# Kernel optimization log

Measured on AMD Instinct MI355X. Metric: run time of the kernel, lower is better.

The kernel has to match this reference:

```python
import jax, jax.numpy as jnp
import numpy as np

S, B, L, D, H, NOP = 4, 8, 512, 128, 128, 64  # segments, batch, seg_len, input_dim, hidden, n_operators
W = S * L  # 2048 total words
FT = 0.1   # forget-gate floor


def _norm_mat(m):
    # divide each row by its count of nonzero entries (torch normalize_matrix)
    cnt = (m != 0).sum(-1, keepdims=True).astype(m.dtype)
    return m / (cnt + 1e-30)


def _l2(x):
    return x / (jnp.linalg.norm(x, axis=-1, keepdims=True) + 1e-30)


def setup_inputs() -> dict:
    key = jax.random.key(0)
    ks = jax.random.split(key, 16)
    word_outputs = jax.random.normal(ks[0], (S, B, L, D), jnp.float32)
    node_hidden = jax.random.normal(ks[1], (B, D), jnp.float32)
    op_embedding = jax.random.normal(ks[2], (B, NOP, D), jnp.float32)
    word_operator = (jax.random.uniform(ks[3], (B, W, NOP)) < 0.05).astype(jnp.float32)
    word_word = (jax.random.uniform(ks[4], (B, W, W)) < 0.02).astype(jnp.float32)
    depend_relation = (jax.random.uniform(ks[5], (S, B, L, L)) < 0.05).astype(jnp.float32)
    word_exist_matrix = (jax.random.uniform(ks[6], (B, W, W)) < 0.9).astype(jnp.float32)
    word_exist_sequence = (jax.random.uniform(ks[7], (B, W)) < 0.9).astype(jnp.float32)
    goal_word = (jax.random.uniform(ks[8], (B, W)) < 0.2).astype(jnp.float32)

    def lin(k, fi, fo):
        k1, k2 = jax.random.split(k)
        s = 1.0 / np.sqrt(fi).astype(np.float32)
        return (jax.random.uniform(k1, (fi, fo), jnp.float32, -s, s),
                jax.random.uniform(k2, (fo,), jnp.float32, -s, s))

    o_w_W, o_w_b = lin(ks[9], D, H)
    wk_W, wk_b = lin(ks[10], D, H)
    ws_W, ws_b = lin(ks[11], D, H)
    up_W, up_b = lin(ks[12], 3 * H, D)
    wg_W, wg_b = lin(ks[13], D, D)
    fg_W, fg_b = lin(ks[14], 2 * D, D)
    return dict(word_outputs=word_outputs, node_hidden=node_hidden, op_embedding=op_embedding,
                word_operator=word_operator, word_word=word_word, depend_relation=depend_relation,
                word_exist_matrix=word_exist_matrix, word_exist_sequence=word_exist_sequence,
                goal_word=goal_word, o_w_W=o_w_W, o_w_b=o_w_b, wk_W=wk_W, wk_b=wk_b,
                ws_W=ws_W, ws_b=ws_b, up_W=up_W, up_b=up_b, wg_W=wg_W, wg_b=wg_b,
                fg_W=fg_W, fg_b=fg_b)


def reference(word_outputs, node_hidden, op_embedding, word_operator, word_word,
              depend_relation, word_exist_matrix, word_exist_sequence, goal_word,
              o_w_W, o_w_b, wk_W, wk_b, ws_W, ws_b, up_W, up_b, wg_W, wg_b, fg_W, fg_b):
    # cat(word_outputs, dim=1) -> [B, W, D]
    all_word = word_outputs.transpose(1, 0, 2, 3).reshape(B, W, D)
    # operator aggregation: [B,W,NOP] @ o_w(op_embedding) -> [B,W,H], L2-normalized
    word_o = _l2(jnp.einsum('bwo,boh->bwh', word_operator, op_embedding @ o_w_W + o_w_b))
    # knowledge aggregation over masked word-word adjacency
    adj_k = _norm_mat(word_word * word_exist_matrix)
    word_w_k = _l2(jnp.einsum('bvw,bwh->bvh', adj_k, all_word @ wk_W + wk_b))
    # per-segment dependency aggregation, then concat along word dim
    seg = jnp.einsum('sbij,sbjh->sbih', _norm_mat(depend_relation), word_outputs @ ws_W + ws_b)
    word_w_s = _l2(seg.transpose(1, 0, 2, 3).reshape(B, W, H))
    neighbor = jnp.concatenate([word_o, word_w_k, word_w_s], axis=-1)  # [B, W, 3H]
    word_updated = jax.nn.relu(neighbor @ up_W + up_b)  # [B, W, D]
    # goal pooling: bmm([B,1,W],[B,W,D]) -> [B,D]
    gw = _norm_mat(goal_word * word_exist_sequence)
    goal_w = jnp.einsum('bw,bwd->bd', gw, word_updated)
    goal_updated = jax.nn.relu(goal_w @ wg_W + wg_b)
    forget = jax.nn.sigmoid(jnp.concatenate([goal_w, node_hidden], axis=-1) @ fg_W + fg_b)
    return jnp.maximum(forget, FT) * node_hidden + (1.0 - forget) * goal_updated
```

## Files before the change

### kernel.cpp

```cpp
#include <hip/hip_runtime.h>
#include <math.h>

#define Sn 4
#define Bn 8
#define Ln 512
#define Dn 128
#define Hn 128
#define NOPn 64
#define Wn 2048


__device__ __forceinline__ float bf2f(unsigned short u) {
    return __uint_as_float(((unsigned int)u) << 16);
}
__device__ __forceinline__ unsigned short f2bf(float f) {
    unsigned int u = __float_as_uint(f);
    return (unsigned short)((u + 0x7FFFu + ((u >> 16) & 1u)) >> 16);
}

__global__ __launch_bounds__(256) void prep_k(const float* __restrict__ A,
                                              const float* __restrict__ W1,
                                              const float* __restrict__ W2,
                                              const float* __restrict__ b1,
                                              const float* __restrict__ b2,
                                              unsigned short* __restrict__ C1,
                                              unsigned short* __restrict__ C2,
                                              const float* __restrict__ ope,
                                              const float* __restrict__ owW,
                                              const float* __restrict__ owb,
                                              unsigned short* __restrict__ oph,
                                              const float* __restrict__ goal,
                                              const float* __restrict__ wes,
                                              int* __restrict__ widx,
                                              int* __restrict__ wcnt,
                                              float* __restrict__ gwacc) {
    __shared__ __align__(16) float lA[32][68];
    __shared__ __align__(16) float lW1[32][132];
    __shared__ __align__(16) float lW2[32][132];
    __shared__ int cnt;
    const int bid = blockIdx.x, tid = threadIdx.x;

    if (bid < 256) {
        const int m0 = bid * 64;
        float acc1[4][8] = {}, acc2[4][8] = {};
        const int r0 = (tid & 15) * 4;
        const int h0 = (tid >> 4) * 8;
        for (int k0 = 0; k0 < 128; k0 += 32) {
            __syncthreads();
            {
                const int r = tid >> 2, kk = (tid & 3) * 8;
                const float* src = A + (size_t)(m0 + r) * 128 + (k0 + kk);
                float4 v0 = reinterpret_cast<const float4*>(src)[0];
                float4 v1 = reinterpret_cast<const float4*>(src)[1];
                lA[kk + 0][r] = v0.x; lA[kk + 1][r] = v0.y;
                lA[kk + 2][r] = v0.z; lA[kk + 3][r] = v0.w;
                lA[kk + 4][r] = v1.x; lA[kk + 5][r] = v1.y;
                lA[kk + 6][r] = v1.z; lA[kk + 7][r] = v1.w;
            }
            {
                const int kk = tid >> 3, hh = (tid & 7) * 16;
                const float* s1 = W1 + (size_t)(k0 + kk) * 128 + hh;
                const float* s2 = W2 + (size_t)(k0 + kk) * 128 + hh;
#pragma unroll
                for (int q = 0; q < 4; ++q) {
                    float4 v1 = reinterpret_cast<const float4*>(s1)[q];
                    float4 v2 = reinterpret_cast<const float4*>(s2)[q];
                    lW1[kk][hh + 4 * q + 0] = v1.x; lW1[kk][hh + 4 * q + 1] = v1.y;
                    lW1[kk][hh + 4 * q + 2] = v1.z; lW1[kk][hh + 4 * q + 3] = v1.w;
                    lW2[kk][hh + 4 * q + 0] = v2.x; lW2[kk][hh + 4 * q + 1] = v2.y;
                    lW2[kk][hh + 4 * q + 2] = v2.z; lW2[kk][hh + 4 * q + 3] = v2.w;
                }
            }
            __syncthreads();
#pragma unroll
            for (int k = 0; k < 32; ++k) {
                float4 a   = *reinterpret_cast<const float4*>(&lA[k][r0]);
                float4 w10 = *reinterpret_cast<const float4*>(&lW1[k][h0]);
                float4 w11 = *reinterpret_cast<const float4*>(&lW1[k][h0 + 4]);
                float4 w20 = *reinterpret_cast<const float4*>(&lW2[k][h0]);
                float4 w21 = *reinterpret_cast<const float4*>(&lW2[k][h0 + 4]);
                float av[4] = {a.x, a.y, a.z, a.w};
                float wv1[8] = {w10.x, w10.y, w10.z, w10.w, w11.x, w11.y, w11.z, w11.w};
                float wv2[8] = {w20.x, w20.y, w20.z, w20.w, w21.x, w21.y, w21.z, w21.w};
#pragma unroll
                for (int i = 0; i < 4; ++i)
#pragma unroll
                    for (int j = 0; j < 8; ++j) {
                        acc1[i][j] = fmaf(av[i], wv1[j], acc1[i][j]);
                        acc2[i][j] = fmaf(av[i], wv2[j], acc2[i][j]);
                    }
            }
        }
#pragma unroll
        for (int i = 0; i < 4; ++i) {
            alignas(16) unsigned short u1[8], u2[8];
#pragma unroll
            for (int j = 0; j < 8; ++j) {
                u1[j] = f2bf(acc1[i][j] + b1[h0 + j]);
                u2[j] = f2bf(acc2[i][j] + b2[h0 + j]);
            }
            const size_t off = (size_t)(m0 + r0 + i) * 128 + h0;
            *reinterpret_cast<uint4*>(C1 + off) = *reinterpret_cast<const uint4*>(u1);
            *reinterpret_cast<uint4*>(C2 + off) = *reinterpret_cast<const uint4*>(u2);
        }
    } else if (bid < 264) {
        const int m0 = (bid - 256) * 64;
        float acc[4][8] = {};
        const int r0 = (tid & 15) * 4;
        const int h0 = (tid >> 4) * 8;
        for (int k0 = 0; k0 < 128; k0 += 32) {
            __syncthreads();
            {
                const int r = tid >> 2, kk = (tid & 3) * 8;
                const float* src = ope + (size_t)(m0 + r) * 128 + (k0 + kk);
                float4 v0 = reinterpret_cast<const float4*>(src)[0];
                float4 v1 = reinterpret_cast<const float4*>(src)[1];
                lA[kk + 0][r] = v0.x; lA[kk + 1][r] = v0.y;
                lA[kk + 2][r] = v0.z; lA[kk + 3][r] = v0.w;
                lA[kk + 4][r] = v1.x; lA[kk + 5][r] = v1.y;
                lA[kk + 6][r] = v1.z; lA[kk + 7][r] = v1.w;
            }
            {
                const int kk = tid >> 3, hh = (tid & 7) * 16;
                const float* src = owW + (size_t)(k0 + kk) * 128 + hh;
#pragma unroll
                for (int q = 0; q < 4; ++q) {
                    float4 v = reinterpret_cast<const float4*>(src)[q];
                    lW1[kk][hh + 4 * q + 0] = v.x; lW1[kk][hh + 4 * q + 1] = v.y;
                    lW1[kk][hh + 4 * q + 2] = v.z; lW1[kk][hh + 4 * q + 3] = v.w;
                }
            }
            __syncthreads();
#pragma unroll
            for (int k = 0; k < 32; ++k) {
                float4 a  = *reinterpret_cast<const float4*>(&lA[k][r0]);
                float4 w0 = *reinterpret_cast<const float4*>(&lW1[k][h0]);
                float4 w1 = *reinterpret_cast<const float4*>(&lW1[k][h0 + 4]);
                float av[4] = {a.x, a.y, a.z, a.w};
                float wv[8] = {w0.x, w0.y, w0.z, w0.w, w1.x, w1.y, w1.z, w1.w};
#pragma unroll
                for (int i = 0; i < 4; ++i)
#pragma unroll
                    for (int j = 0; j < 8; ++j) acc[i][j] = fmaf(av[i], wv[j], acc[i][j]);
            }
        }
#pragma unroll
        for (int i = 0; i < 4; ++i) {
            alignas(16) unsigned short us[8];
#pragma unroll
            for (int j = 0; j < 8; ++j) us[j] = f2bf(acc[i][j] + owb[h0 + j]);
            *reinterpret_cast<uint4*>(oph + (size_t)(m0 + r0 + i) * 128 + h0) =
                *reinterpret_cast<const uint4*>(us);
        }
    } else if (bid < 272) {
        const int b = bid - 264;
        if (tid == 0) cnt = 0;
        __syncthreads();
#pragma unroll
        for (int j = 0; j < 8; ++j) {
            const int w = tid * 8 + j;
            if (goal[b * Wn + w] != 0.f && wes[b * Wn + w] != 0.f) {
                const int p = atomicAdd(&cnt, 1);
                if (p < 1024) widx[b * 1024 + p] = w;
            }
        }
        __syncthreads();
        if (tid == 0) wcnt[b] = cnt < 1024 ? cnt : 1024;
    } else {
        for (int idx = tid; idx < 1024; idx += 256) gwacc[idx] = 0.f;
    }
}

__global__ __launch_bounds__(256) void mega_agg2(const int* __restrict__ widx,
                                                 const int* __restrict__ wcnt,
                                                 const float* __restrict__ ww,
                                                 const float* __restrict__ wem,
                                                 const float* __restrict__ dep,
                                                 const float* __restrict__ wop,
                                                 const unsigned short* __restrict__ oph,
                                                 const unsigned short* __restrict__ wkh,
                                                 const unsigned short* __restrict__ wsh,
                                                 const float* __restrict__ upW,
                                                 const float* __restrict__ upb,
                                                 float* __restrict__ gwacc) {
    const int slot = blockIdx.x;
    const int b = slot >> 10, i = slot & 1023;
    if (i >= wcnt[b]) return;
    const int w_dst = widx[slot];
    const int t = threadIdx.x;
    const int lane = t & 63, wv = t >> 6;

    __shared__ int kidx[512];
    __shared__ int keep[512];
    __shared__ int sidx[256];
    __shared__ int kn, sn;
    __shared__ float part1[4][128];
    __shared__ float part2[4][128];
    __shared__ float nbL[384];
    __shared__ float gpart[256];
    if (t == 0) { kn = 0; sn = 0; }
    __syncthreads();

    const float* wwr = ww + ((size_t)(b * Wn + w_dst)) * Wn;
#pragma unroll
    for (int q = 0; q < 2; ++q) {
        const int e0 = q * 1024 + t * 4;
        float4 v = *reinterpret_cast<const float4*>(wwr + e0);
        float vv[4] = {v.x, v.y, v.z, v.w};
#pragma unroll
        for (int j = 0; j < 4; ++j)
            if (vv[j] != 0.f) {
                int p = atomicAdd(&kn, 1);
                if (p < 512) kidx[p] = e0 + j;
            }
    }
    const int sD = w_dst >> 9, lD = w_dst & 511;
    if (t < 128) {
        const float* dr = dep + ((size_t)((sD * Bn + b) * Ln + lD)) * Ln + t * 4;
        float4 v = *reinterpret_cast<const float4*>(dr);
        float vv[4] = {v.x, v.y, v.z, v.w};
#pragma unroll
        for (int j = 0; j < 4; ++j)
            if (vv[j] != 0.f) {
                int p = atomicAdd(&sn, 1);
                if (p < 256) sidx[p] = t * 4 + j;
            }
    }
    float m_op = 0.f;
    if (wv == 3) m_op = wop[((size_t)(b * Wn + w_dst)) * NOPn + lane];
    __syncthreads();

    const int nk = kn < 512 ? kn : 512;
    const int ns = sn < 256 ? sn : 256;
    for (int p = t; p < nk; p += 256)
        keep[p] = (wem[((size_t)(b * Wn + w_dst)) * Wn + kidx[p]] != 0.f) ? 1 : 0;
    __syncthreads();

    {
        float a0 = 0.f, a1 = 0.f;
        for (int p = wv; p < nk; p += 4)
            if (keep[p]) {
                const int w = kidx[p];
                const int s = w >> 9, l = w & 511;
                ushort2 x = *reinterpret_cast<const ushort2*>(
                    wkh + ((size_t)((s * Bn + b) * Ln + l)) * Hn + 2 * lane);
                a0 += bf2f(x.x);
                a1 += bf2f(x.y);
            }
        part1[wv][2 * lane]     = a0;
        part1[wv][2 * lane + 1] = a1;
    }
    {
        const unsigned short* base = wsh + (size_t)((sD * Bn + b) * Ln) * Hn + 2 * lane;
        float a0 = 0.f, a1 = 0.f;
        for (int p = wv; p < ns; p += 4) {
            ushort2 x = *reinterpret_cast<const ushort2*>(base + (size_t)sidx[p] * Hn);
            a0 += bf2f(x.x);
            a1 += bf2f(x.y);
        }
        part2[wv][2 * lane]     = a0;
        part2[wv][2 * lane + 1] = a1;
    }
    if (wv == 3) {
        unsigned long long bal = __ballot(m_op != 0.f);
        float a0 = 0.f, a1 = 0.f;
        const unsigned short* base = oph + (size_t)b * NOPn * Hn + 2 * lane;
        while (bal) {
            const int o = __ffsll(bal) - 1;
            bal &= bal - 1;
            ushort2 v = *reinterpret_cast<const ushort2*>(base + o * Hn);
            a0 += bf2f(v.x);
            a1 += bf2f(v.y);
        }
        float ss = a0 * a0 + a1 * a1;
#pragma unroll
        for (int off = 1; off < 64; off <<= 1) ss += __shfl_xor(ss, off);
        const float sc = 1.f / (sqrtf(ss) + 1e-30f);
        nbL[2 * lane]     = a0 * sc;
        nbL[2 * lane + 1] = a1 * sc;
    }
    __syncthreads();

    if (wv == 0) {
        float s0 = 0.f, s1 = 0.f;
#pragma unroll
        for (int q = 0; q < 4; ++q) {
            s0 += part1[q][2 * lane];
            s1 += part1[q][2 * lane + 1];
        }
        float ss = s0 * s0 + s1 * s1;
#pragma unroll
        for (int off = 1; off < 64; off <<= 1) ss += __shfl_xor(ss, off);
        const float sc = 1.f / (sqrtf(ss) + 1e-30f);
        nbL[128 + 2 * lane]     = s0 * sc;
        nbL[128 + 2 * lane + 1] = s1 * sc;
    } else if (wv == 1) {
        float s0 = 0.f, s1 = 0.f;
#pragma unroll
        for (int q = 0; q < 4; ++q) {
            s0 += part2[q][2 * lane];
            s1 += part2[q][2 * lane + 1];
        }
        float ss = s0 * s0 + s1 * s1;
#pragma unroll
        for (int off = 1; off < 64; off <<= 1) ss += __shfl_xor(ss, off);
        const float sc = 1.f / (sqrtf(ss) + 1e-30f);
        nbL[256 + 2 * lane]     = s0 * sc;
        nbL[256 + 2 * lane + 1] = s1 * sc;
    }
    __syncthreads();

    {
        const int d = t & 127, half = t >> 7;
        float acc = 0.f;
        const float* wp = upW + (size_t)(half * 192) * 128 + d;
#pragma unroll 8
        for (int k = 0; k < 192; ++k)
            acc = fmaf(nbL[half * 192 + k], wp[(size_t)k * 128], acc);
        gpart[t] = acc;
    }
    __syncthreads();
    if (t < 128) {
        const float g = fmaxf(gpart[t] + gpart[t + 128] + upb[t], 0.f);
        atomicAdd(&gwacc[b * 128 + t], g);
    }
}

__global__ __launch_bounds__(128) void final4_k(const int* __restrict__ wcnt,
                                                const float* __restrict__ gwacc,
                                                const float* __restrict__ nh,
                                                const float* __restrict__ wgW,
                                                const float* __restrict__ wgb,
                                                const float* __restrict__ fgW,
                                                const float* __restrict__ fgb,
                                                float* __restrict__ out) {
    const int b = blockIdx.x, t = threadIdx.x;
    __shared__ float gw[Dn], nhs[Dn];
    const float inv = 1.f / ((float)wcnt[b] + 1e-30f);
    gw[t]  = gwacc[b * Dn + t] * inv;
    nhs[t] = nh[b * Dn + t];
    __syncthreads();
    float gu = wgb[t];
    for (int d = 0; d < Dn; ++d) gu = fmaf(gw[d], wgW[d * Dn + t], gu);
    gu = fmaxf(gu, 0.f);
    float fg = fgb[t];
    for (int d = 0; d < Dn; ++d) fg = fmaf(gw[d], fgW[d * Dn + t], fg);
    for (int d = 0; d < Dn; ++d) fg = fmaf(nhs[d], fgW[(Dn + d) * Dn + t], fg);
    const float forget = 1.f / (1.f + expf(-fg));
    out[b * Dn + t] = fmaxf(forget, 0.1f) * nhs[t] + (1.f - forget) * gu;
}

extern "C" void kernel_launch(void* const* d_in, const int* in_sizes, int n_in,
                              void* d_out, int out_size, void* d_ws, size_t ws_size,
                              hipStream_t stream) {
    (void)in_sizes; (void)n_in; (void)out_size; (void)ws_size;
    const float* word_outputs        = (const float*)d_in[0];
    const float* node_hidden         = (const float*)d_in[1];
    const float* op_embedding        = (const float*)d_in[2];
    const float* word_operator       = (const float*)d_in[3];
    const float* word_word           = (const float*)d_in[4];
    const float* depend_relation     = (const float*)d_in[5];
    const float* word_exist_matrix   = (const float*)d_in[6];
    const float* word_exist_sequence = (const float*)d_in[7];
    const float* goal_word           = (const float*)d_in[8];
    const float* o_w_W = (const float*)d_in[9];
    const float* o_w_b = (const float*)d_in[10];
    const float* wk_W  = (const float*)d_in[11];
    const float* wk_b  = (const float*)d_in[12];
    const float* ws_W  = (const float*)d_in[13];
    const float* ws_b  = (const float*)d_in[14];
    const float* up_W  = (const float*)d_in[15];
    const float* up_b  = (const float*)d_in[16];
    const float* wg_W  = (const float*)d_in[17];
    const float* wg_b  = (const float*)d_in[18];
    const float* fg_W  = (const float*)d_in[19];
    const float* fg_b  = (const float*)d_in[20];
    float* out = (float*)d_out;

    char* ws = (char*)d_ws;
    unsigned short* oph = (unsigned short*)(ws + 0);
    unsigned short* wkh = (unsigned short*)(ws + (1u << 20));
    unsigned short* wsh = (unsigned short*)(ws + (5u << 20));
    int* widx           = (int*)(ws + (9u << 20));
    int* wcnt           = (int*)(ws + (9u << 20) + 32768);
    float* gwacc        = (float*)(ws + (9u << 20) + 65536);

    prep_k<<<273, 256, 0, stream>>>(word_outputs, wk_W, ws_W, wk_b, ws_b, wkh, wsh,
                                    op_embedding, o_w_W, o_w_b, oph,
                                    goal_word, word_exist_sequence, widx, wcnt, gwacc);
    mega_agg2<<<8192, 256, 0, stream>>>(widx, wcnt, word_word, word_exist_matrix,
                                        depend_relation, word_operator, oph, wkh, wsh,
                                        up_W, up_b, gwacc);
    final4_k<<<8, 128, 0, stream>>>(wcnt, gwacc, node_hidden,
                                    wg_W, wg_b, fg_W, fg_b, out);
}
```

Baseline: 354.5 us.

## Fuse final gating into aggregation kernel via last-block counter; store up_W in bf16

The separate final kernel is removed. Each aggregation block now increments a global done counter, and the last block to finish computes the goal and forget-gate outputs for all batches, which saves one kernel launch. The prep kernel also converts up_W to bf16 in two extra blocks, so the per-block up-projection reads half the bytes. In exchange, the last block runs the final matvecs serially, every block pays a threadfence and an atomic, and the bf16 weights add rounding error.

```diff
diff --git a/kernel.cpp b/kernel.cpp
--- a/kernel.cpp
+++ b/kernel.cpp
@@ -33,7 +33,10 @@
                                               const float* __restrict__ wes,
                                               int* __restrict__ widx,
                                               int* __restrict__ wcnt,
-                                              float* __restrict__ gwacc) {
+                                              float* __restrict__ gwacc,
+                                              const float* __restrict__ upW,
+                                              unsigned short* __restrict__ upWbf,
+                                              int* __restrict__ done) {
     __shared__ __align__(16) float lA[32][68];
     __shared__ __align__(16) float lW1[32][132];
     __shared__ __align__(16) float lW2[32][132];
@@ -166,8 +169,16 @@
         }
         __syncthreads();
         if (tid == 0) wcnt[b] = cnt < 1024 ? cnt : 1024;
+    } else if (bid == 272) {
+        for (int idx = tid; idx < 1024; idx += 256) gwacc[idx] = 0.f;
+        if (tid == 0) *done = 0;
     } else {
-        for (int idx = tid; idx < 1024; idx += 256) gwacc[idx] = 0.f;
+        const int base = (bid - 273) * 24576;
+        for (int e = base + tid * 4; e < base + 24576; e += 1024) {
+            float4 v = *reinterpret_cast<const float4*>(upW + e);
+            alignas(8) unsigned short u[4] = {f2bf(v.x), f2bf(v.y), f2bf(v.z), f2bf(v.w)};
+            *reinterpret_cast<uint2*>(upWbf + e) = *reinterpret_cast<const uint2*>(u);
+        }
     }
 }
 
@@ -180,174 +191,191 @@
                                                  const unsigned short* __restrict__ oph,
                                                  const unsigned short* __restrict__ wkh,
                                                  const unsigned short* __restrict__ wsh,
-                                                 const float* __restrict__ upW,
+                                                 const unsigned short* __restrict__ upWbf,
                                                  const float* __restrict__ upb,
-                                                 float* __restrict__ gwacc) {
+                                                 float* __restrict__ gwacc,
+                                                 int* __restrict__ done,
+                                                 const float* __restrict__ nh,
+                                                 const float* __restrict__ wgW,
+                                                 const float* __restrict__ wgb,
+                                                 const float* __restrict__ fgW,
+                                                 const float* __restrict__ fgb,
+                                                 float* __restrict__ out) {
     const int slot = blockIdx.x;
     const int b = slot >> 10, i = slot & 1023;
-    if (i >= wcnt[b]) return;
-    const int w_dst = widx[slot];
     const int t = threadIdx.x;
     const int lane = t & 63, wv = t >> 6;
 
     __shared__ int kidx[512];
     __shared__ int keep[512];
     __shared__ int sidx[256];
-    __shared__ int kn, sn;
+    __shared__ int kn, sn, lastFlag;
     __shared__ float part1[4][128];
     __shared__ float part2[4][128];
     __shared__ float nbL[384];
     __shared__ float gpart[256];
-    if (t == 0) { kn = 0; sn = 0; }
-    __syncthreads();
-
-    const float* wwr = ww + ((size_t)(b * Wn + w_dst)) * Wn;
-#pragma unroll
-    for (int q = 0; q < 2; ++q) {
-        const int e0 = q * 1024 + t * 4;
-        float4 v = *reinterpret_cast<const float4*>(wwr + e0);
-        float vv[4] = {v.x, v.y, v.z, v.w};
-#pragma unroll
-        for (int j = 0; j < 4; ++j)
-            if (vv[j] != 0.f) {
-                int p = atomicAdd(&kn, 1);
-                if (p < 512) kidx[p] = e0 + j;
-            }
-    }
-    const int sD = w_dst >> 9, lD = w_dst & 511;
-    if (t < 128) {
-        const float* dr = dep + ((size_t)((sD * Bn + b) * Ln + lD)) * Ln + t * 4;
-        float4 v = *reinterpret_cast<const float4*>(dr);
-        float vv[4] = {v.x, v.y, v.z, v.w};
-#pragma unroll
-        for (int j = 0; j < 4; ++j)
-            if (vv[j] != 0.f) {
-                int p = atomicAdd(&sn, 1);
-                if (p < 256) sidx[p] = t * 4 + j;
-            }
-    }
-    float m_op = 0.f;
-    if (wv == 3) m_op = wop[((size_t)(b * Wn + w_dst)) * NOPn + lane];
-    __syncthreads();
-
-    const int nk = kn < 512 ? kn : 512;
-    const int ns = sn < 256 ? sn : 256;
-    for (int p = t; p < nk; p += 256)
-        keep[p] = (wem[((size_t)(b * Wn + w_dst)) * Wn + kidx[p]] != 0.f) ? 1 : 0;
-    __syncthreads();
-
-    {
-        float a0 = 0.f, a1 = 0.f;
-        for (int p = wv; p < nk; p += 4)
-            if (keep[p]) {
-                const int w = kidx[p];
-                const int s = w >> 9, l = w & 511;
-                ushort2 x = *reinterpret_cast<const ushort2*>(
-                    wkh + ((size_t)((s * Bn + b) * Ln + l)) * Hn + 2 * lane);
+    __shared__ float gwS[8][128];
+
+    if (i < wcnt[b]) {
+        const int w_dst = widx[slot];
+        if (t == 0) { kn = 0; sn = 0; }
+        __syncthreads();
+
+        const float* wwr = ww + ((size_t)(b * Wn + w_dst)) * Wn;
+#pragma unroll
+        for (int q = 0; q < 2; ++q) {
+            const int e0 = q * 1024 + t * 4;
+            float4 v = *reinterpret_cast<const float4*>(wwr + e0);
+            float vv[4] = {v.x, v.y, v.z, v.w};
+#pragma unroll
+            for (int j = 0; j < 4; ++j)
+                if (vv[j] != 0.f) {
+                    int p = atomicAdd(&kn, 1);
+                    if (p < 512) kidx[p] = e0 + j;
+                }
+        }
+        const int sD = w_dst >> 9, lD = w_dst & 511;
+        if (t < 128) {
+            const float* dr = dep + ((size_t)((sD * Bn + b) * Ln + lD)) * Ln + t * 4;
+            float4 v = *reinterpret_cast<const float4*>(dr);
+            float vv[4] = {v.x, v.y, v.z, v.w};
+#pragma unroll
+            for (int j = 0; j < 4; ++j)
+                if (vv[j] != 0.f) {
+                    int p = atomicAdd(&sn, 1);
+                    if (p < 256) sidx[p] = t * 4 + j;
+                }
+        }
+        float m_op = 0.f;
+        if (wv == 3) m_op = wop[((size_t)(b * Wn + w_dst)) * NOPn + lane];
+        __syncthreads();
+
+        const int nk = kn < 512 ? kn : 512;
+        const int ns = sn < 256 ? sn : 256;
+        for (int p = t; p < nk; p += 256)
+            keep[p] = (wem[((size_t)(b * Wn + w_dst)) * Wn + kidx[p]] != 0.f) ? 1 : 0;
+        __syncthreads();
+
+        {
+            float a0 = 0.f, a1 = 0.f;
+            for (int p = wv; p < nk; p += 4)
+                if (keep[p]) {
+                    const int w = kidx[p];
+                    const int s = w >> 9, l = w & 511;
+                    ushort2 x = *reinterpret_cast<const ushort2*>(
+                        wkh + ((size_t)((s * Bn + b) * Ln + l)) * Hn + 2 * lane);
+                    a0 += bf2f(x.x);
+                    a1 += bf2f(x.y);
+                }
+            part1[wv][2 * lane]     = a0;
+            part1[wv][2 * lane + 1] = a1;
+        }
+        {
+            const unsigned short* base = wsh + (size_t)((sD * Bn + b) * Ln) * Hn + 2 * lane;
+            float a0 = 0.f, a1 = 0.f;
+            for (int p = wv; p < ns; p += 4) {
+                ushort2 x = *reinterpret_cast<const ushort2*>(base + (size_t)sidx[p] * Hn);
                 a0 += bf2f(x.x);
                 a1 += bf2f(x.y);
             }
-        part1[wv][2 * lane]     = a0;
-        part1[wv][2 * lane + 1] = a1;
+            part2[wv][2 * lane]     = a0;
+            part2[wv][2 * lane + 1] = a1;
+        }
+        if (wv == 3) {
+            unsigned long long bal = __ballot(m_op != 0.f);
+            float a0 = 0.f, a1 = 0.f;
+            const unsigned short* base = oph + (size_t)b * NOPn * Hn + 2 * lane;
+            while (bal) {
+                const int o = __ffsll(bal) - 1;
+                bal &= bal - 1;
+                ushort2 v = *reinterpret_cast<const ushort2*>(base + o * Hn);
+                a0 += bf2f(v.x);
+                a1 += bf2f(v.y);
+            }
+            float ss = a0 * a0 + a1 * a1;
+#pragma unroll
+            for (int off = 1; off < 64; off <<= 1) ss += __shfl_xor(ss, off);
+            const float sc = 1.f / (sqrtf(ss) + 1e-30f);
+            nbL[2 * lane]     = a0 * sc;
+            nbL[2 * lane + 1] = a1 * sc;
+        }
+        __syncthreads();
+
+        if (wv == 0) {
+            float s0 = 0.f, s1 = 0.f;
+#pragma unroll
+            for (int q = 0; q < 4; ++q) {
+                s0 += part1[q][2 * lane];
+                s1 += part1[q][2 * lane + 1];
+            }
+            float ss = s0 * s0 + s1 * s1;
+#pragma unroll
+            for (int off = 1; off < 64; off <<= 1) ss += __shfl_xor(ss, off);
+            const float sc = 1.f / (sqrtf(ss) + 1e-30f);
+            nbL[128 + 2 * lane]     = s0 * sc;
+            nbL[128 + 2 * lane + 1] = s1 * sc;
+        } else if (wv == 1) {
+            float s0 = 0.f, s1 = 0.f;
+#pragma unroll
+            for (int q = 0; q < 4; ++q) {
+                s0 += part2[q][2 * lane];
+                s1 += part2[q][2 * lane + 1];
+            }
+            float ss = s0 * s0 + s1 * s1;
+#pragma unroll
+            for (int off = 1; off < 64; off <<= 1) ss += __shfl_xor(ss, off);
+            const float sc = 1.f / (sqrtf(ss) + 1e-30f);
+            nbL[256 + 2 * lane]     = s0 * sc;
+            nbL[256 + 2 * lane + 1] = s1 * sc;
+        }
+        __syncthreads();
+
+        {
+            const int d = t & 127, half = t >> 7;
+            float acc = 0.f;
+            const unsigned short* wp = upWbf + (size_t)(half * 192) * 128 + d;
+#pragma unroll 8
+            for (int k = 0; k < 192; ++k)
+                acc = fmaf(nbL[half * 192 + k], bf2f(wp[(size_t)k * 128]), acc);
+            gpart[t] = acc;
+        }
+        __syncthreads();
+        if (t < 128) {
+            const float g = fmaxf(gpart[t] + gpart[t + 128] + upb[t], 0.f);
+            atomicAdd(&gwacc[b * 128 + t], g);
+        }
+        __threadfence();
     }
-    {
-        const unsigned short* base = wsh + (size_t)((sD * Bn + b) * Ln) * Hn + 2 * lane;
-        float a0 = 0.f, a1 = 0.f;
-        for (int p = wv; p < ns; p += 4) {
-            ushort2 x = *reinterpret_cast<const ushort2*>(base + (size_t)sidx[p] * Hn);
-            a0 += bf2f(x.x);
-            a1 += bf2f(x.y);
-        }
-        part2[wv][2 * lane]     = a0;
-        part2[wv][2 * lane + 1] = a1;
-    }
-    if (wv == 3) {
-        unsigned long long bal = __ballot(m_op != 0.f);
-        float a0 = 0.f, a1 = 0.f;
-        const unsigned short* base = oph + (size_t)b * NOPn * Hn + 2 * lane;
-        while (bal) {
-            const int o = __ffsll(bal) - 1;
-            bal &= bal - 1;
-            ushort2 v = *reinterpret_cast<const ushort2*>(base + o * Hn);
-            a0 += bf2f(v.x);
-            a1 += bf2f(v.y);
-        }
-        float ss = a0 * a0 + a1 * a1;
-#pragma unroll
-        for (int off = 1; off < 64; off <<= 1) ss += __shfl_xor(ss, off);
-        const float sc = 1.f / (sqrtf(ss) + 1e-30f);
-        nbL[2 * lane]     = a0 * sc;
-        nbL[2 * lane + 1] = a1 * sc;
+
+    __syncthreads();
+    if (t == 0)
+        lastFlag = (__hip_atomic_fetch_add(done, 1, __ATOMIC_ACQ_REL,
+                                           __HIP_MEMORY_SCOPE_AGENT) == 8191);
+    __syncthreads();
+    if (!lastFlag) return;
+
+    for (int idx = t; idx < 1024; idx += 256) {
+        const int bb = idx >> 7;
+        const float inv = 1.f / ((float)wcnt[bb] + 1e-30f);
+        gwS[bb][idx & 127] =
+            __hip_atomic_load(&gwacc[idx], __ATOMIC_RELAXED, __HIP_MEMORY_SCOPE_AGENT) * inv;
     }
     __syncthreads();
-
-    if (wv == 0) {
-        float s0 = 0.f, s1 = 0.f;
-#pragma unroll
-        for (int q = 0; q < 4; ++q) {
-            s0 += part1[q][2 * lane];
-            s1 += part1[q][2 * lane + 1];
-        }
-        float ss = s0 * s0 + s1 * s1;
-#pragma unroll
-        for (int off = 1; off < 64; off <<= 1) ss += __shfl_xor(ss, off);
-        const float sc = 1.f / (sqrtf(ss) + 1e-30f);
-        nbL[128 + 2 * lane]     = s0 * sc;
-        nbL[128 + 2 * lane + 1] = s1 * sc;
-    } else if (wv == 1) {
-        float s0 = 0.f, s1 = 0.f;
-#pragma unroll
-        for (int q = 0; q < 4; ++q) {
-            s0 += part2[q][2 * lane];
-            s1 += part2[q][2 * lane + 1];
-        }
-        float ss = s0 * s0 + s1 * s1;
-#pragma unroll
-        for (int off = 1; off < 64; off <<= 1) ss += __shfl_xor(ss, off);
-        const float sc = 1.f / (sqrtf(ss) + 1e-30f);
-        nbL[256 + 2 * lane]     = s0 * sc;
-        nbL[256 + 2 * lane + 1] = s1 * sc;
+    const int d = t & 127;
+    for (int bb = (t >> 7); bb < 8; bb += 2) {
+        float gu = wgb[d], fg = fgb[d];
+        for (int k = 0; k < 128; ++k) {
+            const float g = gwS[bb][k];
+            gu = fmaf(g, wgW[k * 128 + d], gu);
+            fg = fmaf(g, fgW[k * 128 + d], fg);
+        }
+        for (int k = 0; k < 128; ++k)
+            fg = fmaf(nh[bb * 128 + k], fgW[(128 + k) * 128 + d], fg);
+        gu = fmaxf(gu, 0.f);
+        const float forget = 1.f / (1.f + expf(-fg));
+        const float nhd = nh[bb * 128 + d];
+        out[bb * 128 + d] = fmaxf(forget, 0.1f) * nhd + (1.f - forget) * gu;
     }
-    __syncthreads();
-
-    {
-        const int d = t & 127, half = t >> 7;
-        float acc = 0.f;
-        const float* wp = upW + (size_t)(half * 192) * 128 + d;
-#pragma unroll 8
-        for (int k = 0; k < 192; ++k)
-            acc = fmaf(nbL[half * 192 + k], wp[(size_t)k * 128], acc);
-        gpart[t] = acc;
-    }
-    __syncthreads();
-    if (t < 128) {
-        const float g = fmaxf(gpart[t] + gpart[t + 128] + upb[t], 0.f);
-        atomicAdd(&gwacc[b * 128 + t], g);
-    }
-}
-
-__global__ __launch_bounds__(128) void final4_k(const int* __restrict__ wcnt,
-                                                const float* __restrict__ gwacc,
-                                                const float* __restrict__ nh,
-                                                const float* __restrict__ wgW,
-                                                const float* __restrict__ wgb,
-                                                const float* __restrict__ fgW,
-                                                const float* __restrict__ fgb,
-                                                float* __restrict__ out) {
-    const int b = blockIdx.x, t = threadIdx.x;
-    __shared__ float gw[Dn], nhs[Dn];
-    const float inv = 1.f / ((float)wcnt[b] + 1e-30f);
-    gw[t]  = gwacc[b * Dn + t] * inv;
-    nhs[t] = nh[b * Dn + t];
-    __syncthreads();
-    float gu = wgb[t];
-    for (int d = 0; d < Dn; ++d) gu = fmaf(gw[d], wgW[d * Dn + t], gu);
-    gu = fmaxf(gu, 0.f);
-    float fg = fgb[t];
-    for (int d = 0; d < Dn; ++d) fg = fmaf(gw[d], fgW[d * Dn + t], fg);
-    for (int d = 0; d < Dn; ++d) fg = fmaf(nhs[d], fgW[(Dn + d) * Dn + t], fg);
-    const float forget = 1.f / (1.f + expf(-fg));
-    out[b * Dn + t] = fmaxf(forget, 0.1f) * nhs[t] + (1.f - forget) * gu;
 }
 
 extern "C" void kernel_launch(void* const* d_in, const int* in_sizes, int n_in,
@@ -378,19 +406,21 @@
     float* out = (float*)d_out;
 
     char* ws = (char*)d_ws;
-    unsigned short* oph = (unsigned short*)(ws + 0);
-    unsigned short* wkh = (unsigned short*)(ws + (1u << 20));
-    unsigned short* wsh = (unsigned short*)(ws + (5u << 20));
-    int* widx           = (int*)(ws + (9u << 20));
-    int* wcnt           = (int*)(ws + (9u << 20) + 32768);
-    float* gwacc        = (float*)(ws + (9u << 20) + 65536);
-
-    prep_k<<<273, 256, 0, stream>>>(word_outputs, wk_W, ws_W, wk_b, ws_b, wkh, wsh,
+    unsigned short* oph   = (unsigned short*)(ws + 0);
+    unsigned short* wkh   = (unsigned short*)(ws + (1u << 20));
+    unsigned short* wsh   = (unsigned short*)(ws + (5u << 20));
+    int* widx             = (int*)(ws + (9u << 20));
+    int* wcnt             = (int*)(ws + (9u << 20) + 32768);
+    float* gwacc          = (float*)(ws + (9u << 20) + 65536);
+    int* done             = (int*)(ws + (9u << 20) + 69632);
+    unsigned short* upWbf = (unsigned short*)(ws + (9u << 20) + 131072);
+
+    prep_k<<<275, 256, 0, stream>>>(word_outputs, wk_W, ws_W, wk_b, ws_b, wkh, wsh,
                                     op_embedding, o_w_W, o_w_b, oph,
-                                    goal_word, word_exist_sequence, widx, wcnt, gwacc);
+                                    goal_word, word_exist_sequence, widx, wcnt, gwacc,
+                                    up_W, upWbf, done);
     mega_agg2<<<8192, 256, 0, stream>>>(widx, wcnt, word_word, word_exist_matrix,
                                         depend_relation, word_operator, oph, wkh, wsh,
-                                        up_W, up_b, gwacc);
-    final4_k<<<8, 128, 0, stream>>>(wcnt, gwacc, node_hidden,
-                                    wg_W, wg_b, fg_W, fg_b, out);
+                                        upWbf, up_b, gwacc, done,
+                                        node_hidden, wg_W, wg_b, fg_W, fg_b, out);
 }
```

New measurement: 829.1 us. +133.9%, slower.
